# Kernel tuning notes

Measured on AMD Instinct MI355X. Metric: run time of the kernel, lower is better.

The kernel has to match this reference:

```python
import jax, jax.numpy as jnp
import numpy as np

NUM_NEURONS = 4_000_000
NUM_WEIGHTS = 8
SRC_SIZE = 2_000_000


def setup_inputs() -> dict:
    key = jax.random.key(0)
    k1, k2, k3, k4, k5, k6 = jax.random.split(key, 6)
    values_a = jax.random.normal(k1, (SRC_SIZE,), dtype=jnp.float32)
    values_b = jax.random.normal(k2, (SRC_SIZE,), dtype=jnp.float32)
    weights = jax.random.normal(k3, (NUM_WEIGHTS,), dtype=jnp.float32)
    idx_a = jax.random.randint(k4, (SRC_SIZE,), 0, SRC_SIZE, dtype=jnp.int64 if jax.config.jax_enable_x64 else jnp.int32).astype(jnp.int32)
    idx_b = jax.random.randint(k5, (SRC_SIZE,), 0, SRC_SIZE).astype(jnp.int32)
    concat_idx = jax.random.randint(k6, (NUM_NEURONS * NUM_WEIGHTS,), 0, 2 * SRC_SIZE).astype(jnp.int32)
    return {
        "values_a": values_a,
        "values_b": values_b,
        "weights": weights,
        "idx_a": idx_a,
        "idx_b": idx_b,
        "concat_idx": concat_idx,
    }


def reference(values_a, values_b, weights, idx_a, idx_b, concat_idx):
    # GatherModule stage 1: per-source-layer gather of needed ordinals, concatenated
    # in layer order.  [2*SRC_SIZE]
    layer_inputs_needed = jnp.concatenate([values_a[idx_a], values_b[idx_b]])
    # GatherModule stage 2: one entry per (neuron, input) pair.  [NUM_NEURONS*NUM_WEIGHTS]
    gathered = layer_inputs_needed[concat_idx]
    # WeightedRuleLayer: per-input-position weights shared across all neurons,
    # weighted sum over rule-body inputs + tanh activation.  [NUM_NEURONS]
    g = gathered.reshape(-1, weights.shape[0])
    return jnp.tanh(jnp.einsum("nk,k->n", g, weights))
```

## Files before the change

### kernel.cpp

```cpp
#include <hip/hip_runtime.h>
#include <hip/hip_fp16.h>

constexpr int SRC = 2000000;
constexpr int NN  = 4000000;
constexpr int TBL = 2 * SRC;
constexpr int HALF_TBL = TBL / 2;

typedef int v4i __attribute__((ext_vector_type(4)));

__global__ __launch_bounds__(256) void build_half(
    const float* __restrict__ v, const int* __restrict__ idx,
    __half* __restrict__ tout)
{
    const int groups = SRC / 16;
    const int stride = gridDim.x * blockDim.x;
    for (int i = blockIdx.x * blockDim.x + threadIdx.x; i < groups; i += stride) {
        const int base = i * 16;
        v4i c0 = __builtin_nontemporal_load(reinterpret_cast<const v4i*>(idx + base));
        v4i c1 = __builtin_nontemporal_load(reinterpret_cast<const v4i*>(idx + base + 4));
        v4i c2 = __builtin_nontemporal_load(reinterpret_cast<const v4i*>(idx + base + 8));
        v4i c3 = __builtin_nontemporal_load(reinterpret_cast<const v4i*>(idx + base + 12));
        float f0 = v[c0.x], f1 = v[c0.y], f2 = v[c0.z], f3 = v[c0.w];
        float f4 = v[c1.x], f5 = v[c1.y], f6 = v[c1.z], f7 = v[c1.w];
        float f8 = v[c2.x], f9 = v[c2.y], fa = v[c2.z], fb = v[c2.w];
        float fc = v[c3.x], fd = v[c3.y], fe = v[c3.z], ff = v[c3.w];
        #define PK(lo, hi) ((unsigned)__half_as_ushort(__float2half_rn(lo)) \
                          | ((unsigned)__half_as_ushort(__float2half_rn(hi)) << 16))
        uint4 o0 = { PK(f0, f1), PK(f2, f3), PK(f4, f5), PK(f6, f7) };
        uint4 o1 = { PK(f8, f9), PK(fa, fb), PK(fc, fd), PK(fe, ff) };
        #undef PK
        reinterpret_cast<uint4*>(tout + base)[0] = o0;
        reinterpret_cast<uint4*>(tout + base)[1] = o1;
    }
}

template<int PHASE>
__global__ __launch_bounds__(256) void neuron_pass(
    const int*    __restrict__ cidx,
    const __half* __restrict__ table,
    const float*  __restrict__ w,
    float*        __restrict__ po)
{
    float wk[8];
    #pragma unroll
    for (int k = 0; k < 8; ++k) wk[k] = w[k];

    const int tid    = blockIdx.x * blockDim.x + threadIdx.x;
    const int stride = gridDim.x * blockDim.x;

    for (int n = tid; n < NN; n += 2 * stride) {
        const int n2   = n + stride;
        const bool has2 = (n2 < NN);
        const int m2   = has2 ? n2 : n;

        const v4i* pa = reinterpret_cast<const v4i*>(cidx) + (size_t)n  * 2;
        const v4i* pb = reinterpret_cast<const v4i*>(cidx) + (size_t)m2 * 2;
        v4i a0 = __builtin_nontemporal_load(pa);
        v4i a1 = __builtin_nontemporal_load(pa + 1);
        v4i b0 = __builtin_nontemporal_load(pb);
        v4i b1 = __builtin_nontemporal_load(pb + 1);

        #define SEL(c, k, cc, ww)                                            \
            const bool p_##cc = (PHASE == 0) ? ((c) < HALF_TBL)              \
                                             : ((c) >= HALF_TBL);            \
            const int   cc = p_##cc ? (c) : (PHASE == 0 ? 0 : HALF_TBL);     \
            const float ww = p_##cc ? wk[k] : 0.0f;
        SEL(a0.x, 0, ca0, wa0) SEL(a0.y, 1, ca1, wa1)
        SEL(a0.z, 2, ca2, wa2) SEL(a0.w, 3, ca3, wa3)
        SEL(a1.x, 4, ca4, wa4) SEL(a1.y, 5, ca5, wa5)
        SEL(a1.z, 6, ca6, wa6) SEL(a1.w, 7, ca7, wa7)
        SEL(b0.x, 0, cb0, wb0) SEL(b0.y, 1, cb1, wb1)
        SEL(b0.z, 2, cb2, wb2) SEL(b0.w, 3, cb3, wb3)
        SEL(b1.x, 4, cb4, wb4) SEL(b1.y, 5, cb5, wb5)
        SEL(b1.z, 6, cb6, wb6) SEL(b1.w, 7, cb7, wb7)
        #undef SEL

        const __half ga0 = table[ca0], ga1 = table[ca1], ga2 = table[ca2], ga3 = table[ca3];
        const __half ga4 = table[ca4], ga5 = table[ca5], ga6 = table[ca6], ga7 = table[ca7];
        const __half gb0 = table[cb0], gb1 = table[cb1], gb2 = table[cb2], gb3 = table[cb3];
        const __half gb4 = table[cb4], gb5 = table[cb5], gb6 = table[cb6], gb7 = table[cb7];

        float accA = (PHASE == 0) ? 0.0f : __builtin_nontemporal_load(&po[n]);
        float accB = (PHASE == 0) ? 0.0f : __builtin_nontemporal_load(&po[m2]);

        accA += __half2float(ga0) * wa0 + __half2float(ga1) * wa1
              + __half2float(ga2) * wa2 + __half2float(ga3) * wa3
              + __half2float(ga4) * wa4 + __half2float(ga5) * wa5
              + __half2float(ga6) * wa6 + __half2float(ga7) * wa7;
        accB += __half2float(gb0) * wb0 + __half2float(gb1) * wb1
              + __half2float(gb2) * wb2 + __half2float(gb3) * wb3
              + __half2float(gb4) * wb4 + __half2float(gb5) * wb5
              + __half2float(gb6) * wb6 + __half2float(gb7) * wb7;

        if (PHASE == 0) {
            __builtin_nontemporal_store(accA, &po[n]);
            if (has2) __builtin_nontemporal_store(accB, &po[n2]);
        } else {
            __builtin_nontemporal_store(tanhf(accA), &po[n]);
            if (has2) __builtin_nontemporal_store(tanhf(accB), &po[n2]);
        }
    }
}

__global__ __launch_bounds__(256) void fused_kernel(
    const float* __restrict__ va, const float* __restrict__ vb,
    const int*   __restrict__ ia, const int*   __restrict__ ib,
    const int*   __restrict__ cidx,
    const float* __restrict__ w,
    float* __restrict__ out)
{
    __shared__ float ws[8];
    if (threadIdx.x < 8) ws[threadIdx.x] = w[threadIdx.x];
    __syncthreads();

    const int stride = gridDim.x * blockDim.x;
    for (int n = blockIdx.x * blockDim.x + threadIdx.x; n < NN; n += stride) {
        const int4* p = reinterpret_cast<const int4*>(cidx) + (size_t)n * 2;
        int4 c0 = p[0];
        int4 c1 = p[1];
        int c[8] = {c0.x, c0.y, c0.z, c0.w, c1.x, c1.y, c1.z, c1.w};
        float acc = 0.f;
        #pragma unroll
        for (int k = 0; k < 8; ++k) {
            int ci = c[k];
            float v = (ci < SRC) ? va[ia[ci]] : vb[ib[ci - SRC]];
            acc += v * ws[k];
        }
        out[n] = tanhf(acc);
    }
}

extern "C" void kernel_launch(void* const* d_in, const int* in_sizes, int n_in,
                              void* d_out, int out_size, void* d_ws, size_t ws_size,
                              hipStream_t stream) {
    const float* va   = (const float*)d_in[0];
    const float* vb   = (const float*)d_in[1];
    const float* w    = (const float*)d_in[2];
    const int*   ia   = (const int*)d_in[3];
    const int*   ib   = (const int*)d_in[4];
    const int*   cidx = (const int*)d_in[5];
    float* out = (float*)d_out;

    const size_t table_bytes = (size_t)TBL * sizeof(__half);
    if (ws_size >= table_bytes) {
        __half* table = (__half*)d_ws;
        build_half<<<512, 256, 0, stream>>>(va, ia, table);
        build_half<<<512, 256, 0, stream>>>(vb, ib, table + SRC);
        neuron_pass<0><<<2048, 256, 0, stream>>>(cidx, table, w, out);
        neuron_pass<1><<<2048, 256, 0, stream>>>(cidx, table, w, out);
    } else {
        fused_kernel<<<2048, 256, 0, stream>>>(va, vb, ia, ib, cidx, w, out);
    }
}
```

Measured before the change: 427.4 us.

## Split half-table build into two source-range passes for cache locality

The fp16 table build now runs as two passes per source array. The first pass gathers only indices in the lower half of the source (clamping the others), and the second gathers the upper half and merges with the stored lower-half results. The aim is to keep each pass's random-gather working set (4 MB of source floats) resident in cache instead of thrashing over 8 MB. In exchange, index reads double, the table is written twice and read back once, and twice as many kernels are launched.

Result: no change. 425.7 us (-0.4%).

```diff
diff --git a/kernel.cpp b/kernel.cpp
--- a/kernel.cpp
+++ b/kernel.cpp
@@ -5,32 +5,66 @@
 constexpr int NN  = 4000000;
 constexpr int TBL = 2 * SRC;
 constexpr int HALF_TBL = TBL / 2;
+constexpr int HS = SRC / 2;
 
 typedef int v4i __attribute__((ext_vector_type(4)));
+typedef unsigned int uint;
+typedef uint v4u __attribute__((ext_vector_type(4)));
 
-__global__ __launch_bounds__(256) void build_half(
+__global__ __launch_bounds__(256) void build_lo(
     const float* __restrict__ v, const int* __restrict__ idx,
     __half* __restrict__ tout)
 {
-    const int groups = SRC / 16;
+    const int groups = SRC / 8;
     const int stride = gridDim.x * blockDim.x;
     for (int i = blockIdx.x * blockDim.x + threadIdx.x; i < groups; i += stride) {
-        const int base = i * 16;
+        const int base = i * 8;
         v4i c0 = __builtin_nontemporal_load(reinterpret_cast<const v4i*>(idx + base));
         v4i c1 = __builtin_nontemporal_load(reinterpret_cast<const v4i*>(idx + base + 4));
-        v4i c2 = __builtin_nontemporal_load(reinterpret_cast<const v4i*>(idx + base + 8));
-        v4i c3 = __builtin_nontemporal_load(reinterpret_cast<const v4i*>(idx + base + 12));
-        float f0 = v[c0.x], f1 = v[c0.y], f2 = v[c0.z], f3 = v[c0.w];
-        float f4 = v[c1.x], f5 = v[c1.y], f6 = v[c1.z], f7 = v[c1.w];
-        float f8 = v[c2.x], f9 = v[c2.y], fa = v[c2.z], fb = v[c2.w];
-        float fc = v[c3.x], fd = v[c3.y], fe = v[c3.z], ff = v[c3.w];
-        #define PK(lo, hi) ((unsigned)__half_as_ushort(__float2half_rn(lo)) \
-                          | ((unsigned)__half_as_ushort(__float2half_rn(hi)) << 16))
-        uint4 o0 = { PK(f0, f1), PK(f2, f3), PK(f4, f5), PK(f6, f7) };
-        uint4 o1 = { PK(f8, f9), PK(fa, fb), PK(fc, fd), PK(fe, ff) };
+        int d0 = min(c0.x, HS - 1), d1 = min(c0.y, HS - 1);
+        int d2 = min(c0.z, HS - 1), d3 = min(c0.w, HS - 1);
+        int d4 = min(c1.x, HS - 1), d5 = min(c1.y, HS - 1);
+        int d6 = min(c1.z, HS - 1), d7 = min(c1.w, HS - 1);
+        float f0 = v[d0], f1 = v[d1], f2 = v[d2], f3 = v[d3];
+        float f4 = v[d4], f5 = v[d5], f6 = v[d6], f7 = v[d7];
+        #define PK(lo, hi) ((uint)__half_as_ushort(__float2half_rn(lo)) \
+                          | ((uint)__half_as_ushort(__float2half_rn(hi)) << 16))
+        v4u o = { PK(f0, f1), PK(f2, f3), PK(f4, f5), PK(f6, f7) };
         #undef PK
-        reinterpret_cast<uint4*>(tout + base)[0] = o0;
-        reinterpret_cast<uint4*>(tout + base)[1] = o1;
+        __builtin_nontemporal_store(o, reinterpret_cast<v4u*>(tout) + i);
+    }
+}
+
+__global__ __launch_bounds__(256) void build_hi(
+    const float* __restrict__ v, const int* __restrict__ idx,
+    __half* __restrict__ tout)
+{
+    const int groups = SRC / 8;
+    const int stride = gridDim.x * blockDim.x;
+    for (int i = blockIdx.x * blockDim.x + threadIdx.x; i < groups; i += stride) {
+        const int base = i * 8;
+        v4i c0 = __builtin_nontemporal_load(reinterpret_cast<const v4i*>(idx + base));
+        v4i c1 = __builtin_nontemporal_load(reinterpret_cast<const v4i*>(idx + base + 4));
+        int d0 = max(c0.x, HS), d1 = max(c0.y, HS);
+        int d2 = max(c0.z, HS), d3 = max(c0.w, HS);
+        int d4 = max(c1.x, HS), d5 = max(c1.y, HS);
+        int d6 = max(c1.z, HS), d7 = max(c1.w, HS);
+        float f0 = v[d0], f1 = v[d1], f2 = v[d2], f3 = v[d3];
+        float f4 = v[d4], f5 = v[d5], f6 = v[d6], f7 = v[d7];
+        v4u prior = __builtin_nontemporal_load(reinterpret_cast<const v4u*>(tout) + i);
+        #define HB(f) ((uint)__half_as_ushort(__float2half_rn(f)))
+        uint h0 = (c0.x < HS) ? (prior.x & 0xFFFFu)  : HB(f0);
+        uint h1 = (c0.y < HS) ? (prior.x >> 16)      : HB(f1);
+        uint h2 = (c0.z < HS) ? (prior.y & 0xFFFFu)  : HB(f2);
+        uint h3 = (c0.w < HS) ? (prior.y >> 16)      : HB(f3);
+        uint h4 = (c1.x < HS) ? (prior.z & 0xFFFFu)  : HB(f4);
+        uint h5 = (c1.y < HS) ? (prior.z >> 16)      : HB(f5);
+        uint h6 = (c1.z < HS) ? (prior.w & 0xFFFFu)  : HB(f6);
+        uint h7 = (c1.w < HS) ? (prior.w >> 16)      : HB(f7);
+        #undef HB
+        v4u o = { h0 | (h1 << 16), h2 | (h3 << 16),
+                  h4 | (h5 << 16), h6 | (h7 << 16) };
+        __builtin_nontemporal_store(o, reinterpret_cast<v4u*>(tout) + i);
     }
 }
 
@@ -144,8 +178,10 @@
     const size_t table_bytes = (size_t)TBL * sizeof(__half);
     if (ws_size >= table_bytes) {
         __half* table = (__half*)d_ws;
-        build_half<<<512, 256, 0, stream>>>(va, ia, table);
-        build_half<<<512, 256, 0, stream>>>(vb, ib, table + SRC);
+        build_lo<<<1024, 256, 0, stream>>>(va, ia, table);
+        build_hi<<<1024, 256, 0, stream>>>(va, ia, table);
+        build_lo<<<1024, 256, 0, stream>>>(vb, ib, table + SRC);
+        build_hi<<<1024, 256, 0, stream>>>(vb, ib, table + SRC);
         neuron_pass<0><<<2048, 256, 0, stream>>>(cidx, table, w, out);
         neuron_pass<1><<<2048, 256, 0, stream>>>(cidx, table, w, out);
     } else {
```
